# Optimization experiments

Measured on AMD Instinct MI355X. Metric: run time of the kernel, lower is better.

Reference implementation:

```python
import jax, jax.numpy as jnp
import numpy as np

D_MODEL = 1024
N_HEADS = 16
HEAD_DIM = D_MODEL // N_HEADS


def setup_inputs() -> dict:
    key = jax.random.key(0)
    ks = jax.random.split(key, 5)
    s_in = 1.0 / np.sqrt(D_MODEL)
    x = jax.random.normal(ks[0], (4, 2048, D_MODEL), dtype=jnp.float32)
    w_qkv = jax.random.uniform(ks[1], (3 * D_MODEL, D_MODEL), dtype=jnp.float32, minval=-s_in, maxval=s_in)
    b_qkv = jax.random.uniform(ks[2], (3 * D_MODEL,), dtype=jnp.float32, minval=-s_in, maxval=s_in)
    w_out = jax.random.uniform(ks[3], (D_MODEL, D_MODEL), dtype=jnp.float32, minval=-s_in, maxval=s_in)
    b_out = jax.random.uniform(ks[4], (D_MODEL,), dtype=jnp.float32, minval=-s_in, maxval=s_in)
    return {"x": x, "w_qkv": w_qkv, "b_qkv": b_qkv, "w_out": w_out, "b_out": b_out}


def reference(x, w_qkv, b_qkv, w_out, b_out):
    B, T, D = x.shape
    H, hd = N_HEADS, HEAD_DIM
    qkv = x @ w_qkv.T + b_qkv                      # [B, T, 3D]
    q, k, v = jnp.split(qkv, 3, axis=-1)
    # [B, H, T, hd]
    q = q.reshape(B, T, H, hd).transpose(0, 2, 1, 3)
    k = k.reshape(B, T, H, hd).transpose(0, 2, 1, 3)
    v = v.reshape(B, T, H, hd).transpose(0, 2, 1, 3)
    scale = 1.0 / np.sqrt(hd).astype(np.float32)
    attn = jnp.einsum('bhqd,bhkd->bhqk', q, k) * scale
    causal = jnp.triu(jnp.ones((T, T), dtype=bool), k=1)
    attn = jnp.where(causal, -jnp.inf, attn)
    attn = jax.nn.softmax(attn, axis=-1)
    out = jnp.einsum('bhqk,bhkd->bhqd', attn, v)
    out = out.transpose(0, 2, 1, 3).reshape(B, T, D)
    return out @ w_out.T + b_out
```

## Files before the change

### kernel.cpp

```cpp
#include <hip/hip_runtime.h>
#include <hip/hip_bf16.h>
#include <stdint.h>

#define D_MODEL 1024
#define NHEADS 16
#define HD 64
#define BB 4
#define TT 2048
#define MM (BB*TT)
#define NQKV (3*D_MODEL)
#define KK D_MODEL

typedef __attribute__((ext_vector_type(4))) float f32x4;
typedef __attribute__((ext_vector_type(8))) short bf16x8;

__device__ __forceinline__ unsigned short f2bf(float x){
    union { __hip_bfloat16 h; unsigned short u; } c;
    c.h = __float2bfloat16(x);
    return c.u;
}

__device__ __forceinline__ void gload_lds16(const void* g, void* l){
    __builtin_amdgcn_global_load_lds(
        (const __attribute__((address_space(1))) unsigned int*)g,
        (__attribute__((address_space(3))) unsigned int*)l,
        16, 0, 0);
}

#define N4_X  (MM*KK/4)
#define N4_WQ (NQKV*KK/4)
#define N4_WO (D_MODEL*D_MODEL/4)
__global__ void cast3_kernel(const float* __restrict__ x, const float* __restrict__ wq,
                             const float* __restrict__ wo,
                             unsigned short* __restrict__ xb, unsigned short* __restrict__ wqb,
                             unsigned short* __restrict__ wob){
    int i = blockIdx.x * blockDim.x + threadIdx.x;
    const float* src; unsigned short* dst; int j;
    if (i < N4_X)              { src = x;  dst = xb;  j = i; }
    else if (i < N4_X + N4_WQ) { src = wq; dst = wqb; j = i - N4_X; }
    else                       { src = wo; dst = wob; j = i - N4_X - N4_WQ; }
    float4 v = reinterpret_cast<const float4*>(src)[j];
    ushort4 o;
    o.x = f2bf(v.x); o.y = f2bf(v.y); o.z = f2bf(v.z); o.w = f2bf(v.w);
    reinterpret_cast<ushort4*>(dst)[j] = o;
}

__device__ __forceinline__ void gemm_core(
    const unsigned short* __restrict__ A_, const unsigned short* __restrict__ B_,
    int bm, int bn, char* AsL, char* BsL, f32x4 (&acc)[4][4], int tid)
{
    const int w = tid >> 6, l = tid & 63;
    const int wm = w >> 2, wn = w & 3;
    const int lr = l & 15, hi = l >> 4;

    const int swz = ((tid & 7) ^ ((tid >> 3) & 7)) * 8;
    const unsigned short* Ag = A_ + (size_t)(bm + (tid >> 3)) * KK + swz;
    const unsigned short* Bg = B_ + (size_t)(bn + (tid >> 3)) * KK + swz;

    const int rowA = (wm*64 + lr) * 128;
    const int rowB = (wn*64 + lr) * 128;
    const int ck0 = ((0 + hi) ^ (lr & 7)) * 16;
    const int ck1 = ((4 + hi) ^ (lr & 7)) * 16;

    #pragma unroll
    for (int tt = 0; tt < 2; tt++) {
        const size_t k0 = (size_t)tt * 64;
        gload_lds16(Ag + k0,                   AsL + tt*16384 + tid*16);
        gload_lds16(Ag + (size_t)64*KK + k0,   AsL + tt*16384 + 8192 + tid*16);
        #pragma unroll
        for (int j = 0; j < 4; j++)
            gload_lds16(Bg + (size_t)j*64*KK + k0, BsL + tt*32768 + j*8192 + tid*16);
    }

    bf16x8 bfr[4][2];
    for (int t = 0; t < 16; ++t) {
        const int c  = t % 3;
        const int bi = (t + 2) % 3;
        const bool doissue = (t < 14);
        const size_t k2 = (size_t)(t + 2) * 64;
        if (t < 15) asm volatile("s_waitcnt vmcnt(6)" ::: "memory");
        else        asm volatile("s_waitcnt vmcnt(0)" ::: "memory");
        __builtin_amdgcn_s_barrier();
        const char* Ac = AsL + c*16384;
        const char* Bc = BsL + c*32768;
        #pragma unroll
        for (int p = 0; p < 4; p++) {
            bf16x8 a0 = *reinterpret_cast<const bf16x8*>(Ac + rowA + p*2048 + ck0);
            bf16x8 a1 = *reinterpret_cast<const bf16x8*>(Ac + rowA + p*2048 + ck1);
            if (p == 0) {
                #pragma unroll
                for (int n = 0; n < 4; n++) {
                    bfr[n][0] = *reinterpret_cast<const bf16x8*>(Bc + rowB + n*2048 + ck0);
                    bfr[n][1] = *reinterpret_cast<const bf16x8*>(Bc + rowB + n*2048 + ck1);
                }
            }
            if (doissue) {
                if (p == 0) {
                    gload_lds16(Ag + k2,                 AsL + bi*16384 + tid*16);
                    gload_lds16(Ag + (size_t)64*KK + k2, AsL + bi*16384 + 8192 + tid*16);
                } else if (p == 1) {
                    gload_lds16(Bg + k2,                  BsL + bi*32768 + tid*16);
                    gload_lds16(Bg + (size_t)64*KK + k2,  BsL + bi*32768 + 8192 + tid*16);
                } else if (p == 2) {
                    gload_lds16(Bg + (size_t)128*KK + k2, BsL + bi*32768 + 16384 + tid*16);
                    gload_lds16(Bg + (size_t)192*KK + k2, BsL + bi*32768 + 24576 + tid*16);
                }
            }
            __builtin_amdgcn_s_barrier();
            __builtin_amdgcn_s_setprio(1);
            #pragma unroll
            for (int n = 0; n < 4; n++)
                acc[p][n] = __builtin_amdgcn_mfma_f32_16x16x32_bf16(a0, bfr[n][0], acc[p][n], 0, 0, 0);
            #pragma unroll
            for (int n = 0; n < 4; n++)
                acc[p][n] = __builtin_amdgcn_mfma_f32_16x16x32_bf16(a1, bfr[n][1], acc[p][n], 0, 0, 0);
            __builtin_amdgcn_s_setprio(0);
            __builtin_amdgcn_s_barrier();
        }
    }
}

__global__ __launch_bounds__(512, 2) void gemm_qkv(
    const unsigned short* __restrict__ A, const unsigned short* __restrict__ Bw,
    const float* __restrict__ bias,
    unsigned short* __restrict__ qb, unsigned short* __restrict__ kb,
    unsigned short* __restrict__ vtb)
{
    __shared__ alignas(16) unsigned short As[3][128*64];
    __shared__ alignas(16) unsigned short Bs[3][256*64];
    const int tiles_n = NQKV/256;
    int nwg = gridDim.x;
    int orig = blockIdx.x;
    int bid = (orig & 7) * (nwg >> 3) + (orig >> 3);
    int bm = (bid / tiles_n) * 128;
    int bn = (bid % tiles_n) * 256;

    f32x4 acc[4][4] = {};
    gemm_core(A, Bw, bm, bn, (char*)&As[0][0], (char*)&Bs[0][0], acc, threadIdx.x);

    const int tid = threadIdx.x;
    const int w = tid >> 6, l = tid & 63;
    const int wm = w >> 2, wn = w & 3;
    const int lr = l & 15, hi = l >> 4;
    #pragma unroll
    for (int m = 0; m < 4; m++) {
        int gm = bm + wm*64 + m*16 + hi*4;
        int b  = gm >> 11;
        int t  = gm & 2047;
        #pragma unroll
        for (int n = 0; n < 4; n++) {
            int gn = bn + wn*64 + n*16 + lr;
            float bv = bias[gn];
            int sec = gn >> 10;
            int nn  = gn & 1023;
            int h = nn >> 6, d = nn & 63;
            int bh = b * NHEADS + h;
            if (sec == 2) {
                ushort4 pk;
                pk.x = f2bf(acc[m][n][0] + bv);
                pk.y = f2bf(acc[m][n][1] + bv);
                pk.z = f2bf(acc[m][n][2] + bv);
                pk.w = f2bf(acc[m][n][3] + bv);
                *reinterpret_cast<ushort4*>(&vtb[((size_t)bh*HD + d)*TT + t]) = pk;
            } else {
                unsigned short* dst = (sec == 0) ? qb : kb;
                #pragma unroll
                for (int r = 0; r < 4; r++)
                    dst[((size_t)bh*TT + t + r)*HD + d] = f2bf(acc[m][n][r] + bv);
            }
        }
    }
}

__global__ __launch_bounds__(512, 2) void gemm_out(
    const unsigned short* __restrict__ A, const unsigned short* __restrict__ Bw,
    const float* __restrict__ bias, float* __restrict__ out)
{
    __shared__ alignas(16) unsigned short As[3][128*64];
    __shared__ alignas(16) unsigned short Bs[3][256*64];
    const int tiles_n = D_MODEL/256;
    int nwg = gridDim.x;
    int orig = blockIdx.x;
    int bid = (orig & 7) * (nwg >> 3) + (orig >> 3);
    int bm = (bid / tiles_n) * 128;
    int bn = (bid % tiles_n) * 256;

    f32x4 acc[4][4] = {};
    gemm_core(A, Bw, bm, bn, (char*)&As[0][0], (char*)&Bs[0][0], acc, threadIdx.x);

    const int tid = threadIdx.x;
    const int w = tid >> 6, l = tid & 63;
    const int wm = w >> 2, wn = w & 3;
    const int lr = l & 15, hi = l >> 4;
    #pragma unroll
    for (int m = 0; m < 4; m++) {
        int gm = bm + wm*64 + m*16 + hi*4;
        #pragma unroll
        for (int n = 0; n < 4; n++) {
            int gn = bn + wn*64 + n*16 + lr;
            float bv = bias[gn];
            #pragma unroll
            for (int r = 0; r < 4; r++)
                out[(size_t)(gm + r)*D_MODEL + gn] = acc[m][n][r] + bv;
        }
    }
}

__global__ __launch_bounds__(512) void attn_kernel(
    const unsigned short* __restrict__ qb, const unsigned short* __restrict__ kb,
    const unsigned short* __restrict__ vtb, unsigned short* __restrict__ ao)
{
    __shared__ alignas(16) unsigned short Kt[4][64*64];
    __shared__ alignas(16) unsigned short Vt[4][64*64];
    __shared__ alignas(16) unsigned short Pl[8][16*64];

    const int bh = blockIdx.x;
    const int qt = (gridDim.y - 1) - blockIdx.y;
    const int tid = threadIdx.x;
    const int w = tid >> 6, l = tid & 63;
    const int lr = l & 15, hi = l >> 4;

    const int qbase = qt * 128;
    const int qrow  = qbase + w*16;
    const int npairs = qt + 1;

    const unsigned short* Qp = qb + ((size_t)bh*TT + qrow) * HD;
    bf16x8 qf0 = *reinterpret_cast<const bf16x8*>(Qp + lr*HD + hi*8);
    bf16x8 qf1 = *reinterpret_cast<const bf16x8*>(Qp + lr*HD + 32 + hi*8);

    const unsigned short* Kg = kb  + (size_t)bh*TT*HD;
    const unsigned short* Vg = vtb + (size_t)bh*HD*TT;

    const int srow = w*8 + (l >> 3);
    const int sc16 = (l & 7) ^ (srow & 7);
    char* KS0 = (char*)&Kt[0][0] + w*1024;  char* KS1 = (char*)&Kt[1][0] + w*1024;
    char* KS2 = (char*)&Kt[2][0] + w*1024;  char* KS3 = (char*)&Kt[3][0] + w*1024;
    char* VS0 = (char*)&Vt[0][0] + w*1024;  char* VS1 = (char*)&Vt[1][0] + w*1024;
    char* VS2 = (char*)&Vt[2][0] + w*1024;  char* VS3 = (char*)&Vt[3][0] + w*1024;

    gload_lds16(Kg + (size_t)srow*HD + sc16*8,        KS0);
    gload_lds16(Vg + (size_t)srow*TT + sc16*8,        VS0);
    gload_lds16(Kg + (size_t)(64 + srow)*HD + sc16*8, KS1);
    gload_lds16(Vg + (size_t)srow*TT + 64 + sc16*8,   VS1);
    __syncthreads();

    float mS = -3e38f, lS = 0.f;
    f32x4 o[4] = {};
    const float sc = 0.125f * 1.4426950408889634f;
    const float THR = 8.0f / sc;
    const int qg = qrow + lr;
    const int swp = (lr & 7) << 4;
    char* Pw = (char*)&Pl[w][0];

    for (int j = 0; j < npairs; ++j) {
        const int ph = j & 1;
        const char* Ka = ph ? (const char*)&Kt[2][0] : (const char*)&Kt[0][0];
        const char* Kc = ph ? (const char*)&Kt[3][0] : (const char*)&Kt[1][0];
        const char* Va = ph ? (const char*)&Vt[2][0] : (const char*)&Vt[0][0];
        const char* Vc = ph ? (const char*)&Vt[3][0] : (const char*)&Vt[1][0];
        if (j + 1 < npairs) {
            const int tn = 2*j + 2;
            char* kd0 = ph ? KS0 : KS2;  char* kd1 = ph ? KS1 : KS3;
            char* vd0 = ph ? VS0 : VS2;  char* vd1 = ph ? VS1 : VS3;
            gload_lds16(Kg + (size_t)(tn*64 + srow)*HD + sc16*8,      kd0);
            gload_lds16(Vg + (size_t)srow*TT + tn*64 + sc16*8,        vd0);
            gload_lds16(Kg + (size_t)(tn*64 + 64 + srow)*HD + sc16*8, kd1);
            gload_lds16(Vg + (size_t)srow*TT + tn*64 + 64 + sc16*8,   vd1);
        }
        const int kba = 2*j*64;
        const int kbb = kba + 64;
        const bool cb = (kbb <= qrow + 15);

        f32x4 sa4[4] = {}, sb4[4] = {};
        __builtin_amdgcn_s_setprio(1);
        #pragma unroll
        for (int n = 0; n < 4; n++) {
            int rb = (n*16 + lr) * 128;
            bf16x8 k0 = *reinterpret_cast<const bf16x8*>(Ka + rb + (( 0 + hi*16) ^ swp));
            bf16x8 k1 = *reinterpret_cast<const bf16x8*>(Ka + rb + ((64 + hi*16) ^ swp));
            sa4[n] = __builtin_amdgcn_mfma_f32_16x16x32_bf16(k0, qf0, sa4[n], 0, 0, 0);
            sa4[n] = __builtin_amdgcn_mfma_f32_16x16x32_bf16(k1, qf1, sa4[n], 0, 0, 0);
        }
        if (cb) {
            #pragma unroll
            for (int n = 0; n < 4; n++) {
                int rb = (n*16 + lr) * 128;
                bf16x8 k0 = *reinterpret_cast<const bf16x8*>(Kc + rb + (( 0 + hi*16) ^ swp));
                bf16x8 k1 = *reinterpret_cast<const bf16x8*>(Kc + rb + ((64 + hi*16) ^ swp));
                sb4[n] = __builtin_amdgcn_mfma_f32_16x16x32_bf16(k0, qf0, sb4[n], 0, 0, 0);
                sb4[n] = __builtin_amdgcn_mfma_f32_16x16x32_bf16(k1, qf1, sb4[n], 0, 0, 0);
            }
        }
        __builtin_amdgcn_s_setprio(0);

        if (kba + 63 > qrow) {
            #pragma unroll
            for (int n = 0; n < 4; n++)
                #pragma unroll
                for (int r = 0; r < 4; r++)
                    if (kba + n*16 + hi*4 + r > qg) sa4[n][r] = -3e38f;
        }
        if (cb && kbb + 63 > qrow) {
            #pragma unroll
            for (int n = 0; n < 4; n++)
                #pragma unroll
                for (int r = 0; r < 4; r++)
                    if (kbb + n*16 + hi*4 + r > qg) sb4[n][r] = -3e38f;
        }

        float t0 = fmaxf(fmaxf(sa4[0][0], sa4[0][1]), fmaxf(sa4[0][2], sa4[0][3]));
        float t1 = fmaxf(fmaxf(sa4[1][0], sa4[1][1]), fmaxf(sa4[1][2], sa4[1][3]));
        float t2 = fmaxf(fmaxf(sa4[2][0], sa4[2][1]), fmaxf(sa4[2][2], sa4[2][3]));
        float t3 = fmaxf(fmaxf(sa4[3][0], sa4[3][1]), fmaxf(sa4[3][2], sa4[3][3]));
        float rm = fmaxf(fmaxf(t0, t1), fmaxf(t2, t3));
        if (cb) {
            float u0 = fmaxf(fmaxf(sb4[0][0], sb4[0][1]), fmaxf(sb4[0][2], sb4[0][3]));
            float u1 = fmaxf(fmaxf(sb4[1][0], sb4[1][1]), fmaxf(sb4[1][2], sb4[1][3]));
            float u2 = fmaxf(fmaxf(sb4[2][0], sb4[2][1]), fmaxf(sb4[2][2], sb4[2][3]));
            float u3 = fmaxf(fmaxf(sb4[3][0], sb4[3][1]), fmaxf(sb4[3][2], sb4[3][3]));
            rm = fmaxf(rm, fmaxf(fmaxf(u0, u1), fmaxf(u2, u3)));
        }
        rm = fmaxf(rm, __shfl_xor(rm, 16, 64));
        rm = fmaxf(rm, __shfl_xor(rm, 32, 64));
        if (!__all(rm - mS <= THR)) {
            float newm = fmaxf(mS, rm);
            float al = exp2f(sc * (mS - newm));
            mS = newm;
            lS *= al;
            #pragma unroll
            for (int r = 0; r < 4; r++) {
                float alr = __shfl(al, hi*4 + r, 64);
                o[0][r] *= alr; o[1][r] *= alr; o[2][r] *= alr; o[3][r] *= alr;
            }
        }
        const float c0 = sc * mS;

        float rs = 0.f;
        #pragma unroll
        for (int n = 0; n < 4; n++) {
            float p0 = exp2f(fmaf(sa4[n][0], sc, -c0));
            float p1 = exp2f(fmaf(sa4[n][1], sc, -c0));
            float p2 = exp2f(fmaf(sa4[n][2], sc, -c0));
            float p3 = exp2f(fmaf(sa4[n][3], sc, -c0));
            rs += (p0 + p1) + (p2 + p3);
            ushort4 u;
            u.x = f2bf(p0); u.y = f2bf(p1); u.z = f2bf(p2); u.w = f2bf(p3);
            *reinterpret_cast<ushort4*>(Pw + (lr*128 + ((n*32 + hi*8) ^ swp))) = u;
        }
        ushort4 ub[4];
        if (cb) {
            #pragma unroll
            for (int n = 0; n < 4; n++) {
                float p0 = exp2f(fmaf(sb4[n][0], sc, -c0));
                float p1 = exp2f(fmaf(sb4[n][1], sc, -c0));
                float p2 = exp2f(fmaf(sb4[n][2], sc, -c0));
                float p3 = exp2f(fmaf(sb4[n][3], sc, -c0));
                rs += (p0 + p1) + (p2 + p3);
                ub[n].x = f2bf(p0); ub[n].y = f2bf(p1);
                ub[n].z = f2bf(p2); ub[n].w = f2bf(p3);
            }
        }
        rs += __shfl_xor(rs, 16, 64);
        rs += __shfl_xor(rs, 32, 64);
        lS += rs;

        {
            bf16x8 pa0 = *reinterpret_cast<const bf16x8*>(Pw + (lr*128 + (( 0 + hi*16) ^ swp)));
            bf16x8 pa1 = *reinterpret_cast<const bf16x8*>(Pw + (lr*128 + ((64 + hi*16) ^ swp)));
            __builtin_amdgcn_s_setprio(1);
            #pragma unroll
            for (int nd = 0; nd < 4; nd++) {
                int rb = (nd*16 + lr) * 128;
                bf16x8 v0 = *reinterpret_cast<const bf16x8*>(Va + rb + (( 0 + hi*16) ^ swp));
                bf16x8 v1 = *reinterpret_cast<const bf16x8*>(Va + rb + ((64 + hi*16) ^ swp));
                o[nd] = __builtin_amdgcn_mfma_f32_16x16x32_bf16(pa0, v0, o[nd], 0, 0, 0);
                o[nd] = __builtin_amdgcn_mfma_f32_16x16x32_bf16(pa1, v1, o[nd], 0, 0, 0);
            }
            __builtin_amdgcn_s_setprio(0);
        }
        if (cb) {
            #pragma unroll
            for (int n = 0; n < 4; n++)
                *reinterpret_cast<ushort4*>(Pw + (lr*128 + ((n*32 + hi*8) ^ swp))) = ub[n];
            bf16x8 pa0 = *reinterpret_cast<const bf16x8*>(Pw + (lr*128 + (( 0 + hi*16) ^ swp)));
            bf16x8 pa1 = *reinterpret_cast<const bf16x8*>(Pw + (lr*128 + ((64 + hi*16) ^ swp)));
            __builtin_amdgcn_s_setprio(1);
            #pragma unroll
            for (int nd = 0; nd < 4; nd++) {
                int rb = (nd*16 + lr) * 128;
                bf16x8 v0 = *reinterpret_cast<const bf16x8*>(Vc + rb + (( 0 + hi*16) ^ swp));
                bf16x8 v1 = *reinterpret_cast<const bf16x8*>(Vc + rb + ((64 + hi*16) ^ swp));
                o[nd] = __builtin_amdgcn_mfma_f32_16x16x32_bf16(pa0, v0, o[nd], 0, 0, 0);
                o[nd] = __builtin_amdgcn_mfma_f32_16x16x32_bf16(pa1, v1, o[nd], 0, 0, 0);
            }
            __builtin_amdgcn_s_setprio(0);
        }
        __syncthreads();
    }

    float inv = 1.0f / lS;
    int b = bh >> 4, h = bh & 15;
    #pragma unroll
    for (int r = 0; r < 4; r++) {
        float invr = __shfl(inv, hi*4 + r, 64);
        int t = qrow + hi*4 + r;
        #pragma unroll
        for (int nd = 0; nd < 4; nd++) {
            float val = o[nd][r] * invr;
            ao[((size_t)b*TT + t)*D_MODEL + h*HD + nd*16 + lr] = f2bf(val);
        }
    }
}

extern "C" void kernel_launch(void* const* d_in, const int* in_sizes, int n_in,
                              void* d_out, int out_size, void* d_ws, size_t ws_size,
                              hipStream_t stream) {
    const float* x     = (const float*)d_in[0];
    const float* w_qkv = (const float*)d_in[1];
    const float* b_qkv = (const float*)d_in[2];
    const float* w_out = (const float*)d_in[3];
    const float* b_out = (const float*)d_in[4];
    float* out = (float*)d_out;

    char* ws = (char*)d_ws;
    unsigned short* xbf   = (unsigned short*)(ws);
    unsigned short* wqkvb = (unsigned short*)(ws + (size_t)16777216);
    unsigned short* woutb = (unsigned short*)(ws + (size_t)23068672);
    unsigned short* qb    = (unsigned short*)(ws + (size_t)25165824);
    unsigned short* kb    = (unsigned short*)(ws + (size_t)41943040);
    unsigned short* vtb   = (unsigned short*)(ws + (size_t)58720256);
    unsigned short* aob   = xbf;

    cast3_kernel<<<(N4_X + N4_WQ + N4_WO)/256, 256, 0, stream>>>(x, w_qkv, w_out, xbf, wqkvb, woutb);

    gemm_qkv<<<(MM/128)*(NQKV/256), 512, 0, stream>>>(xbf, wqkvb, b_qkv, qb, kb, vtb);
    attn_kernel<<<dim3(BB*NHEADS, TT/128), 512, 0, stream>>>(qb, kb, vtb, aob);
    gemm_out<<<(MM/128)*(D_MODEL/256), 512, 0, stream>>>(aob, woutb, b_out, out);
}
```

Measured before the change: 186.8 us.

## Retile GEMMs to 256x128 blocks with 4 waves and BK=32 pipeline

Reshapes both projection GEMMs from 128x256 tiles with 8 waves and BK=64 to 256x128 tiles with 4 waves and BK=32. Each wave now owns a 128x64 sub-tile with 8x4 accumulators. The inner loop drops the per-subtile barriers and uses one barrier per K step. The LDS layout and swizzle are redone for 32-wide K rows. The aim is more MFMA work per LDS fragment load and less synchronisation, at the cost of twice as many K iterations, higher register pressure and fewer waves to hide latency.

New measurement: 194.3 us. 1.04x slower.

```diff
diff --git a/kernel.cpp b/kernel.cpp
--- a/kernel.cpp
+++ b/kernel.cpp
@@ -47,104 +47,90 @@
 
 __device__ __forceinline__ void gemm_core(
     const unsigned short* __restrict__ A_, const unsigned short* __restrict__ B_,
-    int bm, int bn, char* AsL, char* BsL, f32x4 (&acc)[4][4], int tid)
+    int bm, int bn, char* AsL, char* BsL, f32x4 (&acc)[8][4], int tid)
 {
     const int w = tid >> 6, l = tid & 63;
-    const int wm = w >> 2, wn = w & 3;
+    const int wm = w >> 1, wn = w & 1;
     const int lr = l & 15, hi = l >> 4;
 
-    const int swz = ((tid & 7) ^ ((tid >> 3) & 7)) * 8;
-    const unsigned short* Ag = A_ + (size_t)(bm + (tid >> 3)) * KK + swz;
-    const unsigned short* Bg = B_ + (size_t)(bn + (tid >> 3)) * KK + swz;
-
-    const int rowA = (wm*64 + lr) * 128;
-    const int rowB = (wn*64 + lr) * 128;
-    const int ck0 = ((0 + hi) ^ (lr & 7)) * 16;
-    const int ck1 = ((4 + hi) ^ (lr & 7)) * 16;
+    const int srow = tid >> 2;
+    const int gc16 = (tid & 3) ^ ((tid >> 3) & 3);
+    const unsigned short* Ag = A_ + (size_t)(bm + srow) * KK + gc16*8;
+    const unsigned short* Bg = B_ + (size_t)(bn + srow) * KK + gc16*8;
+
+    const int ck = ((hi ^ ((lr >> 1) & 3)) << 4);
+    const int abase = wm*8192 + lr*64 + ck;
+    const int bbase = wn*4096 + lr*64 + ck;
 
     #pragma unroll
     for (int tt = 0; tt < 2; tt++) {
-        const size_t k0 = (size_t)tt * 64;
-        gload_lds16(Ag + k0,                   AsL + tt*16384 + tid*16);
-        gload_lds16(Ag + (size_t)64*KK + k0,   AsL + tt*16384 + 8192 + tid*16);
-        #pragma unroll
-        for (int j = 0; j < 4; j++)
-            gload_lds16(Bg + (size_t)j*64*KK + k0, BsL + tt*32768 + j*8192 + tid*16);
-    }
-
-    bf16x8 bfr[4][2];
-    for (int t = 0; t < 16; ++t) {
+        const size_t k0 = (size_t)tt * 32;
+        #pragma unroll
+        for (int jj = 0; jj < 4; jj++)
+            gload_lds16(Ag + (size_t)jj*64*KK + k0, AsL + tt*16384 + jj*4096 + tid*16);
+        #pragma unroll
+        for (int jj = 0; jj < 2; jj++)
+            gload_lds16(Bg + (size_t)jj*64*KK + k0, BsL + tt*8192 + jj*4096 + tid*16);
+    }
+
+    for (int t = 0; t < 32; ++t) {
         const int c  = t % 3;
         const int bi = (t + 2) % 3;
-        const bool doissue = (t < 14);
-        const size_t k2 = (size_t)(t + 2) * 64;
-        if (t < 15) asm volatile("s_waitcnt vmcnt(6)" ::: "memory");
+        if (t < 31) asm volatile("s_waitcnt vmcnt(6)" ::: "memory");
         else        asm volatile("s_waitcnt vmcnt(0)" ::: "memory");
         __builtin_amdgcn_s_barrier();
         const char* Ac = AsL + c*16384;
-        const char* Bc = BsL + c*32768;
-        #pragma unroll
-        for (int p = 0; p < 4; p++) {
-            bf16x8 a0 = *reinterpret_cast<const bf16x8*>(Ac + rowA + p*2048 + ck0);
-            bf16x8 a1 = *reinterpret_cast<const bf16x8*>(Ac + rowA + p*2048 + ck1);
-            if (p == 0) {
-                #pragma unroll
-                for (int n = 0; n < 4; n++) {
-                    bfr[n][0] = *reinterpret_cast<const bf16x8*>(Bc + rowB + n*2048 + ck0);
-                    bfr[n][1] = *reinterpret_cast<const bf16x8*>(Bc + rowB + n*2048 + ck1);
-                }
-            }
-            if (doissue) {
-                if (p == 0) {
-                    gload_lds16(Ag + k2,                 AsL + bi*16384 + tid*16);
-                    gload_lds16(Ag + (size_t)64*KK + k2, AsL + bi*16384 + 8192 + tid*16);
-                } else if (p == 1) {
-                    gload_lds16(Bg + k2,                  BsL + bi*32768 + tid*16);
-                    gload_lds16(Bg + (size_t)64*KK + k2,  BsL + bi*32768 + 8192 + tid*16);
-                } else if (p == 2) {
-                    gload_lds16(Bg + (size_t)128*KK + k2, BsL + bi*32768 + 16384 + tid*16);
-                    gload_lds16(Bg + (size_t)192*KK + k2, BsL + bi*32768 + 24576 + tid*16);
-                }
-            }
-            __builtin_amdgcn_s_barrier();
-            __builtin_amdgcn_s_setprio(1);
+        const char* Bc = BsL + c*8192;
+        bf16x8 bfr[4];
+        #pragma unroll
+        for (int n = 0; n < 4; n++)
+            bfr[n] = *reinterpret_cast<const bf16x8*>(Bc + bbase + n*1024);
+        if (t < 30) {
+            const size_t k2 = (size_t)(t + 2) * 32;
+            #pragma unroll
+            for (int jj = 0; jj < 4; jj++)
+                gload_lds16(Ag + (size_t)jj*64*KK + k2, AsL + bi*16384 + jj*4096 + tid*16);
+            #pragma unroll
+            for (int jj = 0; jj < 2; jj++)
+                gload_lds16(Bg + (size_t)jj*64*KK + k2, BsL + bi*8192 + jj*4096 + tid*16);
+        }
+        __builtin_amdgcn_s_setprio(1);
+        #pragma unroll
+        for (int p = 0; p < 8; p++) {
+            bf16x8 af = *reinterpret_cast<const bf16x8*>(Ac + abase + p*1024);
             #pragma unroll
             for (int n = 0; n < 4; n++)
-                acc[p][n] = __builtin_amdgcn_mfma_f32_16x16x32_bf16(a0, bfr[n][0], acc[p][n], 0, 0, 0);
-            #pragma unroll
-            for (int n = 0; n < 4; n++)
-                acc[p][n] = __builtin_amdgcn_mfma_f32_16x16x32_bf16(a1, bfr[n][1], acc[p][n], 0, 0, 0);
-            __builtin_amdgcn_s_setprio(0);
-            __builtin_amdgcn_s_barrier();
-        }
-    }
-}
-
-__global__ __launch_bounds__(512, 2) void gemm_qkv(
+                acc[p][n] = __builtin_amdgcn_mfma_f32_16x16x32_bf16(af, bfr[n], acc[p][n], 0, 0, 0);
+        }
+        __builtin_amdgcn_s_setprio(0);
+    }
+}
+
+__global__ __launch_bounds__(256, 2) void gemm_qkv(
     const unsigned short* __restrict__ A, const unsigned short* __restrict__ Bw,
     const float* __restrict__ bias,
     unsigned short* __restrict__ qb, unsigned short* __restrict__ kb,
     unsigned short* __restrict__ vtb)
 {
-    __shared__ alignas(16) unsigned short As[3][128*64];
-    __shared__ alignas(16) unsigned short Bs[3][256*64];
-    const int tiles_n = NQKV/256;
+    __shared__ alignas(16) unsigned short As[3][256*32];
+    __shared__ alignas(16) unsigned short Bs[3][128*32];
+    const int tiles_n = NQKV/128;
     int nwg = gridDim.x;
     int orig = blockIdx.x;
     int bid = (orig & 7) * (nwg >> 3) + (orig >> 3);
-    int bm = (bid / tiles_n) * 128;
-    int bn = (bid % tiles_n) * 256;
-
-    f32x4 acc[4][4] = {};
+    int bm = (bid / tiles_n) * 256;
+    int bn = (bid % tiles_n) * 128;
+
+    f32x4 acc[8][4] = {};
     gemm_core(A, Bw, bm, bn, (char*)&As[0][0], (char*)&Bs[0][0], acc, threadIdx.x);
 
     const int tid = threadIdx.x;
     const int w = tid >> 6, l = tid & 63;
-    const int wm = w >> 2, wn = w & 3;
+    const int wm = w >> 1, wn = w & 1;
     const int lr = l & 15, hi = l >> 4;
     #pragma unroll
-    for (int m = 0; m < 4; m++) {
-        int gm = bm + wm*64 + m*16 + hi*4;
+    for (int m = 0; m < 8; m++) {
+        int gm = bm + wm*128 + m*16 + hi*4;
         int b  = gm >> 11;
         int t  = gm & 2047;
         #pragma unroll
@@ -172,29 +158,29 @@
     }
 }
 
-__global__ __launch_bounds__(512, 2) void gemm_out(
+__global__ __launch_bounds__(256, 2) void gemm_out(
     const unsigned short* __restrict__ A, const unsigned short* __restrict__ Bw,
     const float* __restrict__ bias, float* __restrict__ out)
 {
-    __shared__ alignas(16) unsigned short As[3][128*64];
-    __shared__ alignas(16) unsigned short Bs[3][256*64];
-    const int tiles_n = D_MODEL/256;
+    __shared__ alignas(16) unsigned short As[3][256*32];
+    __shared__ alignas(16) unsigned short Bs[3][128*32];
+    const int tiles_n = D_MODEL/128;
     int nwg = gridDim.x;
     int orig = blockIdx.x;
     int bid = (orig & 7) * (nwg >> 3) + (orig >> 3);
-    int bm = (bid / tiles_n) * 128;
-    int bn = (bid % tiles_n) * 256;
-
-    f32x4 acc[4][4] = {};
+    int bm = (bid / tiles_n) * 256;
+    int bn = (bid % tiles_n) * 128;
+
+    f32x4 acc[8][4] = {};
     gemm_core(A, Bw, bm, bn, (char*)&As[0][0], (char*)&Bs[0][0], acc, threadIdx.x);
 
     const int tid = threadIdx.x;
     const int w = tid >> 6, l = tid & 63;
-    const int wm = w >> 2, wn = w & 3;
+    const int wm = w >> 1, wn = w & 1;
     const int lr = l & 15, hi = l >> 4;
     #pragma unroll
-    for (int m = 0; m < 4; m++) {
-        int gm = bm + wm*64 + m*16 + hi*4;
+    for (int m = 0; m < 8; m++) {
+        int gm = bm + wm*128 + m*16 + hi*4;
         #pragma unroll
         for (int n = 0; n < 4; n++) {
             int gn = bn + wn*64 + n*16 + lr;
@@ -433,7 +419,7 @@
 
     cast3_kernel<<<(N4_X + N4_WQ + N4_WO)/256, 256, 0, stream>>>(x, w_qkv, w_out, xbf, wqkvb, woutb);
 
-    gemm_qkv<<<(MM/128)*(NQKV/256), 512, 0, stream>>>(xbf, wqkvb, b_qkv, qb, kb, vtb);
+    gemm_qkv<<<(MM/256)*(NQKV/128), 256, 0, stream>>>(xbf, wqkvb, b_qkv, qb, kb, vtb);
     attn_kernel<<<dim3(BB*NHEADS, TT/128), 512, 0, stream>>>(qb, kb, vtb, aob);
-    gemm_out<<<(MM/128)*(D_MODEL/256), 512, 0, stream>>>(aob, woutb, b_out, out);
-}
+    gemm_out<<<(MM/256)*(D_MODEL/128), 256, 0, stream>>>(aob, woutb, b_out, out);
+}
```
